# Performance work log

Measured on AMD Instinct MI355X. Metric: run time of the kernel, lower is better.

The kernel has to match this reference:

```python
import jax, jax.numpy as jnp
import numpy as np

GAMMA = 1.0   # soft-min temperature of the differentiable DP
BIG = 1e9     # stand-in for +inf (keeps vjp NaN-free; underflows to 0 weight in softmin)


def setup_inputs() -> dict:
    key = jax.random.key(0)
    # batched pairwise cost matrix for the alignment DP
    input_array = jax.random.uniform(key, (512, 256, 256), dtype=jnp.float32)
    return {"input_array": input_array}


def reference(input_array):
    """Soft-min alignment DP (edit-distance/soft-DTW style), antidiagonal wavefront.

    D[i,j] = C[i,j] + softmin_gamma(D[i-1,j], D[i,j-1], D[i-1,j-1]); returns D[S-1,S-1].
    Diagonal k holds cells (i, j=k-i); carry = last two diagonals.
    """
    B, S, _ = input_array.shape
    i = jnp.arange(S)
    k = jnp.arange(2 * S - 1)
    js = k[:, None] - i[None, :]                 # [2S-1, S] column index j = k - i
    valid = (js >= 0) & (js < S)                 # which lanes of each diagonal exist
    js_c = jnp.clip(js, 0, S - 1)

    # pack cost diagonals: cd[k, b, i] = C[b, i, k-i]   -> [2S-1, B, S]
    cd = input_array[:, i[None, :], js_c]        # [B, 2S-1, S]
    cd = jnp.transpose(cd, (1, 0, 2))

    d0 = jnp.where(i == 0, cd[0], BIG)           # diagonal k=0: only cell (0,0)
    dm1 = jnp.full((B, S), BIG, input_array.dtype)

    def softmin(stk):                            # stk: [3, B, S]
        return -GAMMA * jax.nn.logsumexp(-stk / GAMMA, axis=0)

    def shift(d):                                # index i -> i-1, pad with BIG
        return jnp.concatenate([jnp.full((B, 1), BIG, d.dtype), d[:, :-1]], axis=1)

    def step(carry, xs):
        d1, d2 = carry                           # diagonals k-1, k-2
        c_k, v_k = xs
        # predecessors of (i, k-i): (i,j-1)->d1[i], (i-1,j)->d1[i-1], (i-1,j-1)->d2[i-1]
        preds = jnp.stack([d1, shift(d1), shift(d2)])
        d = c_k + softmin(preds)
        d = jnp.where(v_k[None, :], d, BIG)
        return (d, d1), None

    (d_last, _), _ = jax.lax.scan(step, (d0, dm1), (cd[1:], valid[1:]))
    return d_last[:, S - 1]                      # D[S-1, S-1] per batch -> [B]
```

## Files before the change

kernel.cpp:

```cpp
#include <hip/hip_runtime.h>

#define S 256
#define L2E 1.44269504088896340736f
#define LN2 0.69314718055994530942f

#define EXP2F(x) __builtin_amdgcn_exp2f(x)
#define LOG2F(x) __builtin_amdgcn_logf(x)


template <int I> __device__ __forceinline__ float comp(const float4& v) {
    if constexpr (I == 0) return v.x;
    else if constexpr (I == 1) return v.y;
    else if constexpr (I == 2) return v.z;
    else return v.w;
}

__device__ __forceinline__ float4 g4f(const float4& v) {
    float4 r;
    r.x = EXP2F(v.x * -L2E); r.y = EXP2F(v.y * -L2E);
    r.z = EXP2F(v.z * -L2E); r.w = EXP2F(v.w * -L2E);
    return r;
}

template <int P, int SB>
__device__ __forceinline__ void stepf(
    int kk, int t, int t4, const float* __restrict__ Cb,
    int rb0, int rb1, int rb2, int rb3,
    float4& c0, float4& c1, float4& c2, float4& c3,
    float4& n0, float4& n1, float4& n2, float4& n3,
    float4& s00, float4& s01, float4& s02, float4& s03,
    float4& s10, float4& s11, float4& s12, float4& s13,
    float4& s20, float4& s21, float4& s22, float4& s23,
    float4& s30, float4& s31, float4& s32, float4& s33,
    float& w10, float& w11, float& w12, float& w13,
    float& w20, float& w21, float& w22, float& w23,
    float& pd1, float& pd2)
{
    const int colr = kk + (20 - P) - t4;
    const int col  = colr < 0 ? 0 : (colr > 252 ? 252 : colr);
    const int rb   = (P == 0) ? rb0 : (P == 1) ? rb1 : (P == 2) ? rb2 : rb3;
    const float4 ld = *(const float4*)(Cb + rb + col);

    float4& cP = (P == 0) ? c0 : (P == 1) ? c1 : (P == 2) ? c2 : c3;
    float4& nP = (P == 0) ? n0 : (P == 1) ? n1 : (P == 2) ? n2 : n3;
    float4& sP =
        (SB == 0) ? ((P == 0) ? s00 : (P == 1) ? s01 : (P == 2) ? s02 : s03)
      : (SB == 1) ? ((P == 0) ? s10 : (P == 1) ? s11 : (P == 2) ? s12 : s13)
      : (SB == 2) ? ((P == 0) ? s20 : (P == 1) ? s21 : (P == 2) ? s22 : s23)
                  : ((P == 0) ? s30 : (P == 1) ? s31 : (P == 2) ? s32 : s33);

    const bool junk = (colr > 268);
    float4 gq;
    gq.x = junk ? 0.0f : EXP2F(sP.x * -L2E);
    gq.y = junk ? 0.0f : EXP2F(sP.y * -L2E);
    gq.z = junk ? 0.0f : EXP2F(sP.z * -L2E);
    gq.w = junk ? 0.0f : EXP2F(sP.w * -L2E);
    cP = nP;
    nP = gq;
    sP = ld;

    const float g0 = comp<(P    ) & 3>(c0);
    const float g1 = comp<(P + 3) & 3>(c1);
    const float g2 = comp<(P + 2) & 3>(c2);
    const float g3 = comp<(P + 1) & 3>(c3);

    const float e0 = g0 * (w10 + pd1 + pd2);
    const float e1 = g1 * (w11 + w10 + w20);
    const float e2 = g2 * (w12 + w11 + w21);
    const float e3 = g3 * (w13 + w12 + w22);

    w20 = w10; w21 = w11; w22 = w12; w23 = w13;
    w10 = e0;  w11 = e1;  w12 = e2;  w13 = e3;

    const float nx = __shfl_up(e3, 1);
    pd2 = pd1;
    pd1 = (t == 0) ? 0.0f : nx;

    asm volatile("" ::: "memory");
}

__global__ __launch_bounds__(64, 1) void dp_softmin_wave(const float* __restrict__ C,
                                                         float* __restrict__ out) {
    const int b = blockIdx.x;
    const int t = threadIdx.x;
    const float* Cb = C + ((size_t)b << 16);
    const int t4 = 4 * t;

    const int rb0 = (t4 + 0) << 8;
    const int rb1 = (t4 + 1) << 8;
    const int rb2 = (t4 + 2) << 8;
    const int rb3 = (t4 + 3) << 8;

    auto cl = [](int c) { return c < 0 ? 0 : (c > 252 ? 252 : c); };
    auto q4 = [&](int rb, int col) { return *(const float4*)(Cb + rb + col); };

    float4 c0 = g4f(q4(rb0, 0)), c1 = g4f(q4(rb1, 0)),
           c2 = g4f(q4(rb2, 0)), c3 = g4f(q4(rb3, 0));
    float4 n0 = g4f(q4(rb0, cl(4 - t4)));
    float4 n1 = c1, n2 = c2, n3 = c3;

    float4 s00 = q4(rb0, cl(20 - t4));
    float4 s01 = q4(rb1, cl(4 - t4));
    float4 s02 = q4(rb2, cl(4 - t4));
    float4 s03 = q4(rb3, cl(4 - t4));
    float4 s10 = q4(rb0, cl(8 - t4)),  s11 = q4(rb1, cl(8 - t4));
    float4 s12 = q4(rb2, cl(8 - t4)),  s13 = q4(rb3, cl(8 - t4));
    float4 s20 = q4(rb0, cl(12 - t4)), s21 = q4(rb1, cl(12 - t4));
    float4 s22 = q4(rb2, cl(12 - t4)), s23 = q4(rb3, cl(12 - t4));
    float4 s30 = q4(rb0, cl(16 - t4)), s31 = q4(rb1, cl(16 - t4));
    float4 s32 = q4(rb2, cl(16 - t4)), s33 = q4(rb3, cl(16 - t4));

    float w10 = 0.0f, w11 = 0.0f, w12 = 0.0f, w13 = 0.0f;
    float w20 = 0.0f, w21 = 0.0f, w22 = 0.0f, w23 = 0.0f;
    float pd1 = 0.0f, pd2 = 0.0f;
    int sig = 0;

    if (t == 0) w10 = c0.x;

    asm volatile("" ::: "memory");

#define ARGS t, t4, Cb, rb0, rb1, rb2, rb3, c0,c1,c2,c3, n0,n1,n2,n3, \
             s00,s01,s02,s03, s10,s11,s12,s13, s20,s21,s22,s23, s30,s31,s32,s33, \
             w10,w11,w12,w13, w20,w21,w22,w23, pd1,pd2

    stepf<1,0>(1, ARGS);  stepf<2,0>(2, ARGS);  stepf<3,0>(3, ARGS);
    stepf<0,1>(4, ARGS);  stepf<1,1>(5, ARGS);  stepf<2,1>(6, ARGS);  stepf<3,1>(7, ARGS);
    stepf<0,2>(8, ARGS);  stepf<1,2>(9, ARGS);  stepf<2,2>(10, ARGS); stepf<3,2>(11, ARGS);
    stepf<0,3>(12, ARGS); stepf<1,3>(13, ARGS); stepf<2,3>(14, ARGS); stepf<3,3>(15, ARGS);

#pragma clang loop unroll(disable)
    for (int kb = 16; kb <= 480; kb += 16) {
        if ((kb & 63) == 0) {
            float M = fmaxf(fmaxf(fmaxf(w10, w11), fmaxf(w12, w13)),
                            fmaxf(fmaxf(w20, w21), fmaxf(w22, w23)));
            #pragma unroll
            for (int m = 1; m < 64; m <<= 1) M = fmaxf(M, __shfl_xor(M, m));
            int e = ((__float_as_int(M) >> 23) & 255) - 127;
            float f = __int_as_float((127 - e) << 23);
            w10 *= f; w11 *= f; w12 *= f; w13 *= f;
            w20 *= f; w21 *= f; w22 *= f; w23 *= f;
            pd1 *= f; pd2 *= f;
            sig -= e;
        }
        stepf<0,0>(kb + 0, ARGS);  stepf<1,0>(kb + 1, ARGS);
        stepf<2,0>(kb + 2, ARGS);  stepf<3,0>(kb + 3, ARGS);
        stepf<0,1>(kb + 4, ARGS);  stepf<1,1>(kb + 5, ARGS);
        stepf<2,1>(kb + 6, ARGS);  stepf<3,1>(kb + 7, ARGS);
        stepf<0,2>(kb + 8, ARGS);  stepf<1,2>(kb + 9, ARGS);
        stepf<2,2>(kb + 10, ARGS); stepf<3,2>(kb + 11, ARGS);
        stepf<0,3>(kb + 12, ARGS); stepf<1,3>(kb + 13, ARGS);
        stepf<2,3>(kb + 14, ARGS); stepf<3,3>(kb + 15, ARGS);
    }

    stepf<0,0>(496, ARGS); stepf<1,0>(497, ARGS); stepf<2,0>(498, ARGS); stepf<3,0>(499, ARGS);
    stepf<0,1>(500, ARGS); stepf<1,1>(501, ARGS); stepf<2,1>(502, ARGS); stepf<3,1>(503, ARGS);
    stepf<0,2>(504, ARGS); stepf<1,2>(505, ARGS); stepf<2,2>(506, ARGS); stepf<3,2>(507, ARGS);
    stepf<0,3>(508, ARGS); stepf<1,3>(509, ARGS); stepf<2,3>(510, ARGS);
#undef ARGS

    if (t == 63) out[b] = ((float)sig - LOG2F(w13)) * LN2;
}

extern "C" void kernel_launch(void* const* d_in, const int* in_sizes, int n_in,
                              void* d_out, int out_size, void* d_ws, size_t ws_size,
                              hipStream_t stream) {
    const float* C = (const float*)d_in[0];
    float* out = (float*)d_out;
    dp_softmin_wave<<<512, 64, 0, stream>>>(C, out);
}
```

Before: 67.58 us.

## Stage cost tiles through LDS with coalesced global loads and ring buffer

Replaces the per-thread strided row loads of the cost matrix (each lane reading a float4 from its own row) with coalesced global loads of 16x16 tiles. These are written into a 64 KB LDS ring buffer and read back per lane in diagonal order one step ahead. The aim is better global-memory coalescing and hiding load latency behind the serial DP chain. The cost is extra LDS traffic and complex index arithmetic whose ordering has no explicit barrier, which is fine only because the block is a single wavefront.

```diff
diff --git a/kernel.cpp b/kernel.cpp
--- a/kernel.cpp
+++ b/kernel.cpp
@@ -1,6 +1,5 @@
 #include <hip/hip_runtime.h>
 
-#define S 256
 #define L2E 1.44269504088896340736f
 #define LN2 0.69314718055994530942f
 
@@ -8,67 +7,72 @@
 #define LOG2F(x) __builtin_amdgcn_logf(x)
 
 
-template <int I> __device__ __forceinline__ float comp(const float4& v) {
+typedef float f4 __attribute__((ext_vector_type(4)));
+
+template <int I> __device__ __forceinline__ float comp(const f4 v) {
     if constexpr (I == 0) return v.x;
     else if constexpr (I == 1) return v.y;
     else if constexpr (I == 2) return v.z;
     else return v.w;
 }
 
-__device__ __forceinline__ float4 g4f(const float4& v) {
-    float4 r;
+__device__ __forceinline__ f4 g4f(const f4 v) {
+    f4 r;
     r.x = EXP2F(v.x * -L2E); r.y = EXP2F(v.y * -L2E);
     r.z = EXP2F(v.z * -L2E); r.w = EXP2F(v.w * -L2E);
     return r;
 }
 
-template <int P, int SB>
+template <int J, bool STAGE, bool RQF>
 __device__ __forceinline__ void stepf(
-    int kk, int t, int t4, const float* __restrict__ Cb,
-    int rb0, int rb1, int rb2, int rb3,
-    float4& c0, float4& c1, float4& c2, float4& c3,
-    float4& n0, float4& n1, float4& n2, float4& n3,
-    float4& s00, float4& s01, float4& s02, float4& s03,
-    float4& s10, float4& s11, float4& s12, float4& s13,
-    float4& s20, float4& s21, float4& s22, float4& s23,
-    float4& s30, float4& s31, float4& s32, float4& s33,
+    int kb, int sg, int sgm1,
+    int t, int t4, int g,
+    const float* __restrict__ Cb, float* lds,
+    int baseR, int glane, int wl0, int wl1, int wl2, int wl3,
+    f4& c0, f4& c1, f4& c2, f4& c3,
+    f4& n0, f4& n1, f4& n2, f4& n3,
+    f4& L0, f4& L1, f4& L2, f4& L3,
+    f4& RQ0, f4& RQ1, f4& RQ2, f4& RQ3,
     float& w10, float& w11, float& w12, float& w13,
     float& w20, float& w21, float& w22, float& w23,
     float& pd1, float& pd2)
 {
-    const int colr = kk + (20 - P) - t4;
-    const int col  = colr < 0 ? 0 : (colr > 252 ? 252 : colr);
-    const int rb   = (P == 0) ? rb0 : (P == 1) ? rb1 : (P == 2) ? rb2 : rb3;
-    const float4 ld = *(const float4*)(Cb + rb + col);
-
-    float4& cP = (P == 0) ? c0 : (P == 1) ? c1 : (P == 2) ? c2 : c3;
-    float4& nP = (P == 0) ? n0 : (P == 1) ? n1 : (P == 2) ? n2 : n3;
-    float4& sP =
-        (SB == 0) ? ((P == 0) ? s00 : (P == 1) ? s01 : (P == 2) ? s02 : s03)
-      : (SB == 1) ? ((P == 0) ? s10 : (P == 1) ? s11 : (P == 2) ? s12 : s13)
-      : (SB == 2) ? ((P == 0) ? s20 : (P == 1) ? s21 : (P == 2) ? s22 : s23)
-                  : ((P == 0) ? s30 : (P == 1) ? s31 : (P == 2) ? s32 : s33);
-
-    const bool junk = (colr > 268);
-    float4 gq;
-    gq.x = junk ? 0.0f : EXP2F(sP.x * -L2E);
-    gq.y = junk ? 0.0f : EXP2F(sP.y * -L2E);
-    gq.z = junk ? 0.0f : EXP2F(sP.z * -L2E);
-    gq.w = junk ? 0.0f : EXP2F(sP.w * -L2E);
+    constexpr int P = J & 3;
+
+    f4& cP  = (P == 0) ? c0 : (P == 1) ? c1 : (P == 2) ? c2 : c3;
+    f4& nP  = (P == 0) ? n0 : (P == 1) ? n1 : (P == 2) ? n2 : n3;
+    f4& LR  = (P == 0) ? L0 : (P == 1) ? L1 : (P == 2) ? L2 : L3;
+    f4& RQP = (P == 0) ? RQ0 : (P == 1) ? RQ1 : (P == 2) ? RQ2 : RQ3;
+
+    const int u  = (kb + J + 4 - P) - t4;
+    const int uc = u < 0 ? 0 : (u > 252 ? 252 : u);
+    const bool ok = (u == uc);
+    f4 gq;
+    gq.x = ok ? EXP2F(RQP.x * -L2E) : 0.0f;
+    gq.y = ok ? EXP2F(RQP.y * -L2E) : 0.0f;
+    gq.z = ok ? EXP2F(RQP.z * -L2E) : 0.0f;
+    gq.w = ok ? EXP2F(RQP.w * -L2E) : 0.0f;
     cP = nP;
     nP = gq;
-    sP = ld;
+
+    if constexpr (STAGE) {
+        constexpr int WG = (J >= 4) ? J - 4 : J + 12;
+        const int wsv = (J >= 4) ? sg : sgm1;
+        int ww = wsv - WG; ww = ww < 0 ? 0 : (ww > 15 ? 15 : ww);
+        const int wlP = (P == 0) ? wl0 : (P == 1) ? wl1 : (P == 2) ? wl2 : wl3;
+        *(f4*)(lds + ((ww & 3) * 16 + WG) * 256 + wlP) = LR;
+        int wl = sg - J; wl = wl < 0 ? 0 : (wl > 15 ? 15 : wl);
+        LR = *(const f4*)(Cb + J * 4096 + wl * 16 + glane);
+    }
 
     const float g0 = comp<(P    ) & 3>(c0);
     const float g1 = comp<(P + 3) & 3>(c1);
     const float g2 = comp<(P + 2) & 3>(c2);
     const float g3 = comp<(P + 1) & 3>(c3);
-
     const float e0 = g0 * (w10 + pd1 + pd2);
     const float e1 = g1 * (w11 + w10 + w20);
     const float e2 = g2 * (w12 + w11 + w21);
     const float e3 = g3 * (w13 + w12 + w22);
-
     w20 = w10; w21 = w11; w22 = w12; w23 = w13;
     w10 = e0;  w11 = e1;  w12 = e2;  w13 = e3;
 
@@ -76,6 +80,15 @@
     pd2 = pd1;
     pd1 = (t == 0) ? 0.0f : nx;
 
+    asm volatile("" ::: "memory");
+
+    if constexpr (RQF) {
+        const int u2  = (kb + J + 8 - P) - t4;
+        const int uc2 = u2 < 0 ? 0 : (u2 > 252 ? 252 : u2);
+        const int s2  = (uc2 >> 4) & 3;
+        const int pq  = ((uc2 >> 2) + g) & 3;
+        RQP = *(const f4*)(lds + s2 * 4096 + baseR + 16 * P + pq * 4);
+    }
     asm volatile("" ::: "memory");
 }
 
@@ -85,48 +98,68 @@
     const int t = threadIdx.x;
     const float* Cb = C + ((size_t)b << 16);
     const int t4 = 4 * t;
-
-    const int rb0 = (t4 + 0) << 8;
-    const int rb1 = (t4 + 1) << 8;
-    const int rb2 = (t4 + 2) << 8;
-    const int rb3 = (t4 + 3) << 8;
+    const int g  = t >> 2;
+
+    __shared__ float ldsmem[16384];
+    float* lds = ldsmem;
+
+    const int baseR = g * 256 + 64 * (t & 3);
+    const int glane = (t >> 2) * 256 + (t & 3) * 4;
+    const int wl0 = (t >> 2) * 16 + (((t & 3) + 0) & 3) * 4;
+    const int wl1 = (t >> 2) * 16 + (((t & 3) + 1) & 3) * 4;
+    const int wl2 = (t >> 2) * 16 + (((t & 3) + 2) & 3) * 4;
+    const int wl3 = (t >> 2) * 16 + (((t & 3) + 3) & 3) * 4;
 
     auto cl = [](int c) { return c < 0 ? 0 : (c > 252 ? 252 : c); };
-    auto q4 = [&](int rb, int col) { return *(const float4*)(Cb + rb + col); };
-
-    float4 c0 = g4f(q4(rb0, 0)), c1 = g4f(q4(rb1, 0)),
-           c2 = g4f(q4(rb2, 0)), c3 = g4f(q4(rb3, 0));
-    float4 n0 = g4f(q4(rb0, cl(4 - t4)));
-    float4 n1 = c1, n2 = c2, n3 = c3;
-
-    float4 s00 = q4(rb0, cl(20 - t4));
-    float4 s01 = q4(rb1, cl(4 - t4));
-    float4 s02 = q4(rb2, cl(4 - t4));
-    float4 s03 = q4(rb3, cl(4 - t4));
-    float4 s10 = q4(rb0, cl(8 - t4)),  s11 = q4(rb1, cl(8 - t4));
-    float4 s12 = q4(rb2, cl(8 - t4)),  s13 = q4(rb3, cl(8 - t4));
-    float4 s20 = q4(rb0, cl(12 - t4)), s21 = q4(rb1, cl(12 - t4));
-    float4 s22 = q4(rb2, cl(12 - t4)), s23 = q4(rb3, cl(12 - t4));
-    float4 s30 = q4(rb0, cl(16 - t4)), s31 = q4(rb1, cl(16 - t4));
-    float4 s32 = q4(rb2, cl(16 - t4)), s33 = q4(rb3, cl(16 - t4));
+    auto q4 = [&](int rb, int col) { return *(const f4*)(Cb + rb + col); };
+    const int rb0 = (t4 + 0) << 8, rb1 = (t4 + 1) << 8,
+              rb2 = (t4 + 2) << 8, rb3 = (t4 + 3) << 8;
+    f4 c0 = g4f(q4(rb0, 0)), c1 = g4f(q4(rb1, 0)),
+       c2 = g4f(q4(rb2, 0)), c3 = g4f(q4(rb3, 0));
+    f4 n0 = g4f(q4(rb0, cl(4 - t4)));
+    f4 n1 = c1, n2 = c2, n3 = c3;
+
+    {
+        f4 a0 = *(const f4*)(Cb + 0 * 4096 + 0 * 16 + glane);
+        f4 a1 = *(const f4*)(Cb + 0 * 4096 + 1 * 16 + glane);
+        f4 a2 = *(const f4*)(Cb + 1 * 4096 + 0 * 16 + glane);
+        *(f4*)(lds + (0 * 16 + 0) * 256 + wl0) = a0;
+        *(f4*)(lds + (1 * 16 + 0) * 256 + wl0) = a1;
+        *(f4*)(lds + (0 * 16 + 1) * 256 + wl1) = a2;
+    }
+
+    f4 L1 = *(const f4*)(Cb + 13 * 4096 + glane);
+    f4 L2 = *(const f4*)(Cb + 14 * 4096 + glane);
+    f4 L3 = *(const f4*)(Cb + 15 * 4096 + glane);
+    f4 L0 = *(const f4*)(Cb + 0 * 4096 + 2 * 16 + glane);
+
+    auto rqpre = [&](int kk, int Pp) -> f4 {
+        int u2  = (kk + 4 - Pp) - t4;
+        int uc2 = u2 < 0 ? 0 : (u2 > 252 ? 252 : u2);
+        int s2  = (uc2 >> 4) & 3;
+        int pq  = ((uc2 >> 2) + g) & 3;
+        return *(const f4*)(lds + s2 * 4096 + baseR + 16 * Pp + pq * 4);
+    };
+    f4 RQ1 = rqpre(1, 1), RQ2 = rqpre(2, 2), RQ3 = rqpre(3, 3), RQ0 = rqpre(4, 0);
 
     float w10 = 0.0f, w11 = 0.0f, w12 = 0.0f, w13 = 0.0f;
     float w20 = 0.0f, w21 = 0.0f, w22 = 0.0f, w23 = 0.0f;
     float pd1 = 0.0f, pd2 = 0.0f;
     int sig = 0;
-
     if (t == 0) w10 = c0.x;
 
-    asm volatile("" ::: "memory");
-
-#define ARGS t, t4, Cb, rb0, rb1, rb2, rb3, c0,c1,c2,c3, n0,n1,n2,n3, \
-             s00,s01,s02,s03, s10,s11,s12,s13, s20,s21,s22,s23, s30,s31,s32,s33, \
+#define ARGS t, t4, g, Cb, lds, baseR, glane, wl0, wl1, wl2, wl3, \
+             c0,c1,c2,c3, n0,n1,n2,n3, L0,L1,L2,L3, RQ0,RQ1,RQ2,RQ3, \
              w10,w11,w12,w13, w20,w21,w22,w23, pd1,pd2
 
-    stepf<1,0>(1, ARGS);  stepf<2,0>(2, ARGS);  stepf<3,0>(3, ARGS);
-    stepf<0,1>(4, ARGS);  stepf<1,1>(5, ARGS);  stepf<2,1>(6, ARGS);  stepf<3,1>(7, ARGS);
-    stepf<0,2>(8, ARGS);  stepf<1,2>(9, ARGS);  stepf<2,2>(10, ARGS); stepf<3,2>(11, ARGS);
-    stepf<0,3>(12, ARGS); stepf<1,3>(13, ARGS); stepf<2,3>(14, ARGS); stepf<3,3>(15, ARGS);
+    stepf< 1,true,true>(0,2,1, ARGS); stepf< 2,true,true>(0,2,1, ARGS);
+    stepf< 3,true,true>(0,2,1, ARGS); stepf< 4,true,true>(0,2,1, ARGS);
+    stepf< 5,true,true>(0,2,1, ARGS); stepf< 6,true,true>(0,2,1, ARGS);
+    stepf< 7,true,true>(0,2,1, ARGS); stepf< 8,true,true>(0,2,1, ARGS);
+    stepf< 9,true,true>(0,2,1, ARGS); stepf<10,true,true>(0,2,1, ARGS);
+    stepf<11,true,true>(0,2,1, ARGS); stepf<12,true,true>(0,2,1, ARGS);
+    stepf<13,true,true>(0,2,1, ARGS); stepf<14,true,true>(0,2,1, ARGS);
+    stepf<15,true,true>(0,2,1, ARGS);
 
 #pragma clang loop unroll(disable)
     for (int kb = 16; kb <= 480; kb += 16) {
@@ -142,20 +175,25 @@
             pd1 *= f; pd2 *= f;
             sig -= e;
         }
-        stepf<0,0>(kb + 0, ARGS);  stepf<1,0>(kb + 1, ARGS);
-        stepf<2,0>(kb + 2, ARGS);  stepf<3,0>(kb + 3, ARGS);
-        stepf<0,1>(kb + 4, ARGS);  stepf<1,1>(kb + 5, ARGS);
-        stepf<2,1>(kb + 6, ARGS);  stepf<3,1>(kb + 7, ARGS);
-        stepf<0,2>(kb + 8, ARGS);  stepf<1,2>(kb + 9, ARGS);
-        stepf<2,2>(kb + 10, ARGS); stepf<3,2>(kb + 11, ARGS);
-        stepf<0,3>(kb + 12, ARGS); stepf<1,3>(kb + 13, ARGS);
-        stepf<2,3>(kb + 14, ARGS); stepf<3,3>(kb + 15, ARGS);
-    }
-
-    stepf<0,0>(496, ARGS); stepf<1,0>(497, ARGS); stepf<2,0>(498, ARGS); stepf<3,0>(499, ARGS);
-    stepf<0,1>(500, ARGS); stepf<1,1>(501, ARGS); stepf<2,1>(502, ARGS); stepf<3,1>(503, ARGS);
-    stepf<0,2>(504, ARGS); stepf<1,2>(505, ARGS); stepf<2,2>(506, ARGS); stepf<3,2>(507, ARGS);
-    stepf<0,3>(508, ARGS); stepf<1,3>(509, ARGS); stepf<2,3>(510, ARGS);
+        const int sg = (kb >> 4) + 2, sgm1 = sg - 1;
+        stepf< 0,true,true>(kb, sg, sgm1, ARGS); stepf< 1,true,true>(kb, sg, sgm1, ARGS);
+        stepf< 2,true,true>(kb, sg, sgm1, ARGS); stepf< 3,true,true>(kb, sg, sgm1, ARGS);
+        stepf< 4,true,true>(kb, sg, sgm1, ARGS); stepf< 5,true,true>(kb, sg, sgm1, ARGS);
+        stepf< 6,true,true>(kb, sg, sgm1, ARGS); stepf< 7,true,true>(kb, sg, sgm1, ARGS);
+        stepf< 8,true,true>(kb, sg, sgm1, ARGS); stepf< 9,true,true>(kb, sg, sgm1, ARGS);
+        stepf<10,true,true>(kb, sg, sgm1, ARGS); stepf<11,true,true>(kb, sg, sgm1, ARGS);
+        stepf<12,true,true>(kb, sg, sgm1, ARGS); stepf<13,true,true>(kb, sg, sgm1, ARGS);
+        stepf<14,true,true>(kb, sg, sgm1, ARGS); stepf<15,true,true>(kb, sg, sgm1, ARGS);
+    }
+
+    stepf< 0,false,true >(496,0,0, ARGS); stepf< 1,false,true >(496,0,0, ARGS);
+    stepf< 2,false,true >(496,0,0, ARGS); stepf< 3,false,true >(496,0,0, ARGS);
+    stepf< 4,false,true >(496,0,0, ARGS); stepf< 5,false,true >(496,0,0, ARGS);
+    stepf< 6,false,true >(496,0,0, ARGS); stepf< 7,false,true >(496,0,0, ARGS);
+    stepf< 8,false,true >(496,0,0, ARGS); stepf< 9,false,true >(496,0,0, ARGS);
+    stepf<10,false,true >(496,0,0, ARGS); stepf<11,false,false>(496,0,0, ARGS);
+    stepf<12,false,false>(496,0,0, ARGS); stepf<13,false,false>(496,0,0, ARGS);
+    stepf<14,false,false>(496,0,0, ARGS);
 #undef ARGS
 
     if (t == 63) out[b] = ((float)sig - LOG2F(w13)) * LN2;
```

New measurement: 70.34 us. +4.1%, slower.
